# Kernel tuning notes

Hardware: AMD Instinct MI355X
Metric: run time of the kernel (lower is better)

Reference implementation:

```python
import jax, jax.numpy as jnp
import numpy as np

B, L, ENC, DEC, ATT = 64, 1024, 1024, 1024, 1024


def setup_inputs() -> dict:
    key = jax.random.key(0)
    ks = jax.random.split(key, 8)
    s1 = 1.0 / np.sqrt(ENC)
    s2 = 1.0 / np.sqrt(DEC)
    s3 = 1.0 / np.sqrt(ATT)
    return {
        "features": jax.random.normal(ks[0], (B, L, ENC), jnp.float32),
        "hidden_state": jax.random.normal(ks[1], (B, DEC), jnp.float32),
        "W1_w": jax.random.uniform(ks[2], (ENC, ATT), jnp.float32, -s1, s1),
        "W1_b": jax.random.uniform(ks[3], (ATT,), jnp.float32, -s1, s1),
        "W2_w": jax.random.uniform(ks[4], (DEC, ATT), jnp.float32, -s2, s2),
        "W2_b": jax.random.uniform(ks[5], (ATT,), jnp.float32, -s2, s2),
        "V_w": jax.random.uniform(ks[6], (ATT,), jnp.float32, -s3, s3),
        "V_b": jax.random.uniform(ks[7], (), jnp.float32, -s3, s3),
    }


def reference(features, hidden_state, W1_w, W1_b, W2_w, W2_b, V_w, V_b):
    # proj_f: [B, L, ATT]; proj_h: [B, 1, ATT]
    proj_f = jnp.einsum('ble,ea->bla', features, W1_w) + W1_b
    proj_h = (hidden_state @ W2_w + W2_b)[:, None, :]
    scores = jnp.tanh(proj_f + proj_h) @ V_w + V_b  # [B, L]
    alpha = jax.nn.softmax(scores, axis=1)
    context = jnp.einsum('bl,ble->be', alpha, features)
    return alpha, context
```

## Files before the change

kernel.cpp:

```cpp
#include <hip/hip_runtime.h>
#include <hip/hip_bf16.h>


typedef __bf16 bf16x8 __attribute__((ext_vector_type(8)));
typedef float floatx4 __attribute__((ext_vector_type(4)));
typedef unsigned short ushort_t;
typedef unsigned long long u64;

__device__ __forceinline__ ushort_t f2b(float x) {
    union { float f; unsigned u; } v; v.f = x;
    unsigned r = (v.u + 0x7fffu + ((v.u >> 16) & 1u)) >> 16;
    return (ushort_t)r;
}

__device__ __forceinline__ u64 pack4(float4 f) {
    return (u64)f2b(f.x) | ((u64)f2b(f.y) << 16) |
           ((u64)f2b(f.z) << 32) | ((u64)f2b(f.w) << 48);
}

__device__ __forceinline__ void gload_lds16(const void* g, void* l) {
    __builtin_amdgcn_global_load_lds(
        (const __attribute__((address_space(1))) void*)g,
        (__attribute__((address_space(3))) void*)l, 16, 0, 0);
}

__device__ __forceinline__ float fast_tanh(float x) {
    const float ax = fabsf(x);
    const float t  = __expf(-2.0f * ax);
    const float r  = (1.0f - t) * __builtin_amdgcn_rcpf(1.0f + t);
    return copysignf(r, x);
}

__global__ __launch_bounds__(256) void convert_feat_kernel(
    const float* __restrict__ feat, ushort_t* __restrict__ featb) {
    const size_t idx = ((size_t)blockIdx.x * 256 + threadIdx.x) * 8;
    const float4 f0 = *(const float4*)(feat + idx);
    const float4 f1 = *(const float4*)(feat + idx + 4);
    *(u64*)(featb + idx)     = pack4(f0);
    *(u64*)(featb + idx + 4) = pack4(f1);
}

__global__ __launch_bounds__(256) void transpose_w1_kernel(
    const float* __restrict__ w1, ushort_t* __restrict__ w1t) {
    __shared__ ushort_t tile[64][65];
    const int k0 = blockIdx.x * 64, n0 = blockIdx.y * 64;
    const int tr = threadIdx.x >> 6;
    const int tc = threadIdx.x & 63;
#pragma unroll
    for (int i = 0; i < 16; i++) {
        int r = i * 4 + tr;
        tile[tc][r] = f2b(w1[(size_t)(k0 + r) * 1024 + n0 + tc]);
    }
    __syncthreads();
#pragma unroll
    for (int i = 0; i < 16; i++) {
        int r = i * 4 + tr;
        w1t[(size_t)(n0 + r) * 1024 + k0 + tc] = tile[r][tc];
    }
}

__global__ __launch_bounds__(256) void projh_kernel(
    const float* __restrict__ hidden, const float* __restrict__ w2,
    const float* __restrict__ w2b, const float* __restrict__ w1b,
    float* __restrict__ ph) {
    const int b  = blockIdx.y;
    const int al = threadIdx.x & 63;
    const int eg = threadIdx.x >> 6;
    const int a  = blockIdx.x * 64 + al;
    const float* h = hidden + b * 1024;
    float sum = 0.f;
    const int e0 = eg * 256;
#pragma unroll 8
    for (int e = e0; e < e0 + 256; e++)
        sum += h[e] * w2[(size_t)e * 1024 + a];
    __shared__ float red[256];
    red[threadIdx.x] = sum;
    __syncthreads();
    if (threadIdx.x < 64)
        ph[b * 1024 + a] = w2b[a] + w1b[a] + red[al] + red[al + 64] +
                           red[al + 128] + red[al + 192];
}

__global__ __launch_bounds__(256) void gemm_scores_bf16_kernel(
    const ushort_t* __restrict__ featb,
    const ushort_t* __restrict__ w1t,
    const float* __restrict__ ph,
    const float* __restrict__ vw,
    float* __restrict__ part) {
    __shared__ ushort_t As[128 * 64];
    __shared__ ushort_t Bs[128 * 64];
    __shared__ float cbias[128];
    __shared__ float vvw[128];

    const int tid = threadIdx.x;
    const int lid = blockIdx.y * 8 + blockIdx.x;
    const int c   = lid & 7;
    const int rr  = lid >> 3;
    const int mt  = (rr >> 3) * 8 + c;
    const int nt  = rr & 7;
    const int n0 = nt * 128;
    const int m0 = mt * 128;
    const int b  = m0 >> 10;

    if (tid < 128) {
        cbias[tid] = ph[(b << 10) + n0 + tid];
        vvw[tid]   = vw[n0 + tid];
    }

    const int wave = tid >> 6;
    const int lane = tid & 63;
    const int wr = (wave >> 1) * 64;
    const int wc = (wave & 1) * 64;
    const int q  = lane >> 4;
    const int l15 = lane & 15;

    floatx4 acc[4][4] = {};

    const int srow = lane >> 3;
    const int scol = ((lane & 7) ^ srow) << 3;

    const ushort_t* aBase = featb + (size_t)m0 * 1024;
    const ushort_t* bBase = w1t  + (size_t)n0 * 1024;

    for (int kt = 0; kt < 1024; kt += 64) {
#pragma unroll
        for (int p = 0; p < 4; p++) {
            const int seg = wave * 4 + p;
            const int row = seg * 8 + srow;
            gload_lds16(aBase + (size_t)row * 1024 + kt + scol, As + seg * 512);
            gload_lds16(bBase + (size_t)row * 1024 + kt + scol, Bs + seg * 512);
        }
        __syncthreads();
#pragma unroll
        for (int ks = 0; ks < 64; ks += 32) {
            bf16x8 af[4], bfr[4];
#pragma unroll
            for (int t = 0; t < 4; t++) {
                const int r = wr + t * 16 + l15;
                const int g = (ks >> 3) + q;
                af[t] = *(const bf16x8*)&As[r * 64 + ((g ^ (r & 7)) << 3)];
            }
#pragma unroll
            for (int t = 0; t < 4; t++) {
                const int r = wc + t * 16 + l15;
                const int g = (ks >> 3) + q;
                bfr[t] = *(const bf16x8*)&Bs[r * 64 + ((g ^ (r & 7)) << 3)];
            }
#pragma unroll
            for (int tm = 0; tm < 4; tm++)
#pragma unroll
                for (int tn = 0; tn < 4; tn++)
                    acc[tm][tn] = __builtin_amdgcn_mfma_f32_16x16x32_bf16(
                        af[tm], bfr[tn], acc[tm][tn], 0, 0, 0);
        }
        __syncthreads();
    }

    const int slot = nt * 2 + (wave & 1);
#pragma unroll
    for (int tm = 0; tm < 4; tm++) {
#pragma unroll
        for (int r = 0; r < 4; r++) {
            const int row = wr + tm * 16 + q * 4 + r;
            float s = 0.f;
#pragma unroll
            for (int tn = 0; tn < 4; tn++) {
                const int col = wc + tn * 16 + l15;
                s += fast_tanh(acc[tm][tn][r] + cbias[col]) * vvw[col];
            }
            s += __shfl_xor(s, 1);
            s += __shfl_xor(s, 2);
            s += __shfl_xor(s, 4);
            s += __shfl_xor(s, 8);
            if (l15 == 0) part[slot * 65536 + m0 + row] = s;
        }
    }
}

__global__ __launch_bounds__(256) void softmax_kernel(
    const float* __restrict__ part, float* __restrict__ alpha) {
    const int b = blockIdx.x;
    const int tid = threadIdx.x;
    __shared__ float red[256];
    float v[4];
    float mx = -1e30f;
#pragma unroll
    for (int i = 0; i < 4; i++) {
        const int m = b * 1024 + tid + i * 256;
        float s = 0.f;
#pragma unroll
        for (int nb = 0; nb < 16; nb++) s += part[nb * 65536 + m];
        v[i] = s;
        mx = fmaxf(mx, s);
    }
    red[tid] = mx; __syncthreads();
    for (int s = 128; s > 0; s >>= 1) {
        if (tid < s) red[tid] = fmaxf(red[tid], red[tid + s]);
        __syncthreads();
    }
    mx = red[0]; __syncthreads();
    float sum = 0.f;
#pragma unroll
    for (int i = 0; i < 4; i++) { v[i] = __expf(v[i] - mx); sum += v[i]; }
    red[tid] = sum; __syncthreads();
    for (int s = 128; s > 0; s >>= 1) {
        if (tid < s) red[tid] += red[tid + s];
        __syncthreads();
    }
    const float inv = 1.0f / red[0];
#pragma unroll
    for (int i = 0; i < 4; i++)
        alpha[b * 1024 + tid + i * 256] = v[i] * inv;
}

__global__ __launch_bounds__(1024) void context_kernel(
    const float* __restrict__ alpha, const float* __restrict__ feat,
    float* __restrict__ ctx) {
    const int b  = blockIdx.y;
    const int el = threadIdx.x & 63;
    const int lg = threadIdx.x >> 6;
    const int e  = blockIdx.x * 256 + el * 4;
    const float* fb = feat + (size_t)b * 1024 * 1024;
    const float* ab = alpha + b * 1024;
    floatx4 acc = {};
    const int l0 = lg * 64;
#pragma unroll 4
    for (int l = l0; l < l0 + 64; l++) {
        const float a = ab[l];
        const floatx4 f = *(const floatx4*)(fb + (size_t)l * 1024 + e);
        acc += a * f;
    }
    __shared__ floatx4 red[16 * 64];
    red[lg * 64 + el] = acc;
    __syncthreads();
#pragma unroll
    for (int s = 8; s > 0; s >>= 1) {
        if (lg < s) red[lg * 64 + el] += red[(lg + s) * 64 + el];
        __syncthreads();
    }
    if (lg == 0)
        *(floatx4*)(ctx + b * 1024 + e) = red[el];
}

#define KP 72
__global__ __launch_bounds__(256) void gemm_scores_f32_kernel(
    const float* __restrict__ feat, const ushort_t* __restrict__ w1t,
    const float* __restrict__ ph, const float* __restrict__ vw,
    float* __restrict__ part) {
    __shared__ ushort_t As[128 * KP];
    __shared__ ushort_t Bs[128 * KP];
    __shared__ float cbias[128];
    __shared__ float vvw[128];
    const int tid = threadIdx.x;
    const int nt = blockIdx.x, n0 = nt * 128, m0 = blockIdx.y * 128;
    const int b = m0 >> 10;
    if (tid < 128) { cbias[tid] = ph[(b << 10) + n0 + tid]; vvw[tid] = vw[n0 + tid]; }
    const int wave = tid >> 6, lane = tid & 63;
    const int wr = (wave >> 1) * 64, wc = (wave & 1) * 64;
    const int q = lane >> 4, l15 = lane & 15;
    floatx4 acc[4][4] = {};
    const int arow = tid >> 4, acol = (tid & 15) * 4;
    const int brow = tid >> 3, bcol = (tid & 7) * 8;
    const float* aptr = feat + (size_t)m0 * 1024;
    const ushort_t* bptr = w1t + (size_t)n0 * 1024;
    for (int kt = 0; kt < 1024; kt += 64) {
#pragma unroll
        for (int p = 0; p < 8; p++) {
            int r = p * 16 + arow;
            const float4 f = *(const float4*)(aptr + (size_t)r * 1024 + kt + acol);
            *(u64*)&As[r * KP + acol] = pack4(f);
        }
#pragma unroll
        for (int p = 0; p < 4; p++) {
            int r = p * 32 + brow;
            *(uint4*)&Bs[r * KP + bcol] =
                *(const uint4*)(bptr + (size_t)r * 1024 + kt + bcol);
        }
        __syncthreads();
#pragma unroll
        for (int ks = 0; ks < 64; ks += 32) {
            bf16x8 af[4], bfr[4];
#pragma unroll
            for (int t = 0; t < 4; t++)
                af[t] = *(const bf16x8*)&As[(wr + t * 16 + l15) * KP + ks + q * 8];
#pragma unroll
            for (int t = 0; t < 4; t++)
                bfr[t] = *(const bf16x8*)&Bs[(wc + t * 16 + l15) * KP + ks + q * 8];
#pragma unroll
            for (int tm = 0; tm < 4; tm++)
#pragma unroll
                for (int tn = 0; tn < 4; tn++)
                    acc[tm][tn] = __builtin_amdgcn_mfma_f32_16x16x32_bf16(
                        af[tm], bfr[tn], acc[tm][tn], 0, 0, 0);
        }
        __syncthreads();
    }
    const int slot = nt * 2 + (wave & 1);
#pragma unroll
    for (int tm = 0; tm < 4; tm++) {
#pragma unroll
        for (int r = 0; r < 4; r++) {
            const int row = wr + tm * 16 + q * 4 + r;
            float s = 0.f;
#pragma unroll
            for (int tn = 0; tn < 4; tn++) {
                const int col = wc + tn * 16 + l15;
                s += fast_tanh(acc[tm][tn][r] + cbias[col]) * vvw[col];
            }
            s += __shfl_xor(s, 1);
            s += __shfl_xor(s, 2);
            s += __shfl_xor(s, 4);
            s += __shfl_xor(s, 8);
            if (l15 == 0) part[slot * 65536 + m0 + row] = s;
        }
    }
}

extern "C" void kernel_launch(void* const* d_in, const int* in_sizes, int n_in,
                              void* d_out, int out_size, void* d_ws, size_t ws_size,
                              hipStream_t stream) {
    const float* feat = (const float*)d_in[0];
    const float* hid  = (const float*)d_in[1];
    const float* w1w  = (const float*)d_in[2];
    const float* w1b  = (const float*)d_in[3];
    const float* w2w  = (const float*)d_in[4];
    const float* w2b  = (const float*)d_in[5];
    const float* vw   = (const float*)d_in[6];

    const size_t FEATB_BYTES = (size_t)64 * 1024 * 1024 * 2;
    const size_t W1T_BYTES   = (size_t)1024 * 1024 * 2;
    const size_t PH_BYTES    = (size_t)64 * 1024 * 4;
    const size_t PART_BYTES  = (size_t)16 * 65536 * 4;
    const bool   big_ws = ws_size >= FEATB_BYTES + W1T_BYTES + PH_BYTES + PART_BYTES;
    if (!big_ws && ws_size < W1T_BYTES + PH_BYTES + PART_BYTES) return;

    char* ws = (char*)d_ws;
    ushort_t* featb = (ushort_t*)ws;
    size_t off = big_ws ? FEATB_BYTES : 0;
    ushort_t* w1t  = (ushort_t*)(ws + off);
    float* ph      = (float*)(ws + off + W1T_BYTES);
    float* part    = (float*)(ws + off + W1T_BYTES + PH_BYTES);

    float* alpha = (float*)d_out;
    float* ctx   = alpha + 64 * 1024;

    transpose_w1_kernel<<<dim3(16, 16), 256, 0, stream>>>(w1w, w1t);
    projh_kernel<<<dim3(16, 64), 256, 0, stream>>>(hid, w2w, w2b, w1b, ph);
    if (big_ws) {
        convert_feat_kernel<<<32768, 256, 0, stream>>>(feat, featb);
        gemm_scores_bf16_kernel<<<dim3(8, 512), 256, 0, stream>>>(
            featb, w1t, ph, vw, part);
    } else {
        gemm_scores_f32_kernel<<<dim3(8, 512), 256, 0, stream>>>(
            feat, w1t, ph, vw, part);
    }
    softmax_kernel<<<64, 256, 0, stream>>>(part, alpha);
    context_kernel<<<dim3(4, 64), 1024, 0, stream>>>(alpha, feat, ctx);
}
```

Before: 672.4 us.

## Read bf16 features in context pass and simplify tanh epilogue algebra

The context reduction now reads the already-converted bf16 feature copy instead of the fp32 original, halving the bytes streamed for that pass. The GEMM epilogue rewrites tanh(x)·v as v − 2v/(1+exp(2x)) using exp2 with a pre-scaled bias, so the per-element sum of v is hoisted and copysign/abs work disappears. LDS fragment offsets are precomputed once outside the k-loop. Using bf16 features for the context sum lowers its precision.

```diff
diff --git a/kernel.cpp b/kernel.cpp
--- a/kernel.cpp
+++ b/kernel.cpp
@@ -11,6 +11,10 @@
     union { float f; unsigned u; } v; v.f = x;
     unsigned r = (v.u + 0x7fffu + ((v.u >> 16) & 1u)) >> 16;
     return (ushort_t)r;
+}
+
+__device__ __forceinline__ float b2f(ushort_t u) {
+    union { unsigned u; float f; } v; v.u = (unsigned)u << 16; return v.f;
 }
 
 __device__ __forceinline__ u64 pack4(float4 f) {
@@ -81,6 +85,8 @@
                            red[al + 128] + red[al + 192];
 }
 
+#define LOG2E2 2.885390082f
+
 __global__ __launch_bounds__(256) void gemm_scores_bf16_kernel(
     const ushort_t* __restrict__ featb,
     const ushort_t* __restrict__ w1t,
@@ -122,6 +128,17 @@
     const ushort_t* aBase = featb + (size_t)m0 * 1024;
     const ushort_t* bBase = w1t  + (size_t)n0 * 1024;
 
+    int aoff[4][2], boff[4][2];
+#pragma unroll
+    for (int t = 0; t < 4; t++) {
+        const int ra = wr + t * 16 + l15;
+        const int rb = wc + t * 16 + l15;
+        aoff[t][0] = ra * 64 + (((q    ) ^ (ra & 7)) << 3);
+        aoff[t][1] = ra * 64 + (((q + 4) ^ (ra & 7)) << 3);
+        boff[t][0] = rb * 64 + (((q    ) ^ (rb & 7)) << 3);
+        boff[t][1] = rb * 64 + (((q + 4) ^ (rb & 7)) << 3);
+    }
+
     for (int kt = 0; kt < 1024; kt += 64) {
 #pragma unroll
         for (int p = 0; p < 4; p++) {
@@ -132,20 +149,12 @@
         }
         __syncthreads();
 #pragma unroll
-        for (int ks = 0; ks < 64; ks += 32) {
+        for (int h = 0; h < 2; h++) {
             bf16x8 af[4], bfr[4];
 #pragma unroll
-            for (int t = 0; t < 4; t++) {
-                const int r = wr + t * 16 + l15;
-                const int g = (ks >> 3) + q;
-                af[t] = *(const bf16x8*)&As[r * 64 + ((g ^ (r & 7)) << 3)];
-            }
-#pragma unroll
-            for (int t = 0; t < 4; t++) {
-                const int r = wc + t * 16 + l15;
-                const int g = (ks >> 3) + q;
-                bfr[t] = *(const bf16x8*)&Bs[r * 64 + ((g ^ (r & 7)) << 3)];
-            }
+            for (int t = 0; t < 4; t++) af[t]  = *(const bf16x8*)&As[aoff[t][h]];
+#pragma unroll
+            for (int t = 0; t < 4; t++) bfr[t] = *(const bf16x8*)&Bs[boff[t][h]];
 #pragma unroll
             for (int tm = 0; tm < 4; tm++)
 #pragma unroll
@@ -156,18 +165,29 @@
         __syncthreads();
     }
 
+    float vv[4], cbk[4];
+    float sum_vvw = 0.f;
+#pragma unroll
+    for (int tn = 0; tn < 4; tn++) {
+        const int col = wc + tn * 16 + l15;
+        vv[tn]  = vvw[col];
+        cbk[tn] = LOG2E2 * cbias[col];
+        sum_vvw += vv[tn];
+    }
     const int slot = nt * 2 + (wave & 1);
 #pragma unroll
     for (int tm = 0; tm < 4; tm++) {
 #pragma unroll
         for (int r = 0; r < 4; r++) {
             const int row = wr + tm * 16 + q * 4 + r;
-            float s = 0.f;
+            float s2 = 0.f;
 #pragma unroll
             for (int tn = 0; tn < 4; tn++) {
-                const int col = wc + tn * 16 + l15;
-                s += fast_tanh(acc[tm][tn][r] + cbias[col]) * vvw[col];
+                const float arg = fmaf(LOG2E2, acc[tm][tn][r], cbk[tn]);
+                const float e   = __builtin_amdgcn_exp2f(arg);
+                s2 = fmaf(__builtin_amdgcn_rcpf(1.0f + e), vv[tn], s2);
             }
+            float s = fmaf(-2.0f, s2, sum_vvw);
             s += __shfl_xor(s, 1);
             s += __shfl_xor(s, 2);
             s += __shfl_xor(s, 4);
@@ -211,6 +231,38 @@
 #pragma unroll
     for (int i = 0; i < 4; i++)
         alpha[b * 1024 + tid + i * 256] = v[i] * inv;
+}
+
+__global__ __launch_bounds__(1024) void context_bf16_kernel(
+    const float* __restrict__ alpha, const ushort_t* __restrict__ featb,
+    float* __restrict__ ctx) {
+    const int b  = blockIdx.y;
+    const int el = threadIdx.x & 63;
+    const int lg = threadIdx.x >> 6;
+    const int e  = blockIdx.x * 256 + el * 4;
+    const ushort_t* fb = featb + ((size_t)b << 20) + e;
+    const float* ab = alpha + b * 1024;
+    floatx4 acc = {};
+    const int l0 = lg * 64;
+#pragma unroll 4
+    for (int l = l0; l < l0 + 64; l++) {
+        const float a = ab[l];
+        const ushort4 u = *(const ushort4*)(fb + (size_t)l * 1024);
+        acc[0] = fmaf(a, b2f(u.x), acc[0]);
+        acc[1] = fmaf(a, b2f(u.y), acc[1]);
+        acc[2] = fmaf(a, b2f(u.z), acc[2]);
+        acc[3] = fmaf(a, b2f(u.w), acc[3]);
+    }
+    __shared__ floatx4 red[16 * 64];
+    red[lg * 64 + el] = acc;
+    __syncthreads();
+#pragma unroll
+    for (int s = 8; s > 0; s >>= 1) {
+        if (lg < s) red[lg * 64 + el] += red[(lg + s) * 64 + el];
+        __syncthreads();
+    }
+    if (lg == 0)
+        *(floatx4*)(ctx + b * 1024 + e) = red[el];
 }
 
 __global__ __launch_bounds__(1024) void context_kernel(
@@ -350,10 +402,12 @@
         convert_feat_kernel<<<32768, 256, 0, stream>>>(feat, featb);
         gemm_scores_bf16_kernel<<<dim3(8, 512), 256, 0, stream>>>(
             featb, w1t, ph, vw, part);
+        softmax_kernel<<<64, 256, 0, stream>>>(part, alpha);
+        context_bf16_kernel<<<dim3(4, 64), 1024, 0, stream>>>(alpha, featb, ctx);
     } else {
         gemm_scores_f32_kernel<<<dim3(8, 512), 256, 0, stream>>>(
             feat, w1t, ph, vw, part);
-    }
-    softmax_kernel<<<64, 256, 0, stream>>>(part, alpha);
-    context_kernel<<<dim3(4, 64), 1024, 0, stream>>>(alpha, feat, ctx);
-}
+        softmax_kernel<<<64, 256, 0, stream>>>(part, alpha);
+        context_kernel<<<dim3(4, 64), 1024, 0, stream>>>(alpha, feat, ctx);
+    }
+}
```

Result: faster. 644.3 us (-4.2%).
